# Kernel optimization log

Hardware: AMD Instinct MI355X
Metric: run time of the kernel (lower is better)

The kernel has to match this reference:

```python
import jax, jax.numpy as jnp
import numpy as np

EPS = 0.0001
N, E, DIN, H, DH, C, G = 50000, 800000, 256, 4, 64, 10, 100


def setup_inputs() -> dict:
    key = jax.random.key(0)
    ks = jax.random.split(key, 10)
    x = jax.random.normal(ks[0], (N, DIN), dtype=jnp.float32)
    src = jax.random.randint(ks[1], (E,), 0, N)
    dst = jax.random.randint(ks[2], (E,), 0, N)
    midx = jnp.stack([src, dst]).astype(jnp.int32)
    batch = jnp.sort(jax.random.randint(ks[3], (N,), 0, G)).astype(jnp.int32)
    W_feat = jax.random.normal(ks[4], (DIN, H * DH), dtype=jnp.float32) / np.sqrt(DIN)
    phi = jax.random.normal(ks[5], (H, 2 * DH, 1), dtype=jnp.float32) / np.sqrt(2 * DH)
    W1 = jax.random.normal(ks[6], (H * DH, DH), dtype=jnp.float32) / np.sqrt(H * DH)
    b1 = jnp.zeros((DH,), jnp.float32)
    W2 = jax.random.normal(ks[7], (DH, C), dtype=jnp.float32) / np.sqrt(DH)
    b2 = jnp.zeros((C,), jnp.float32)
    return {"x": x, "midx": midx, "batch": batch, "W_feat": W_feat,
            "phi": phi, "W1": W1, "b1": b1, "W2": W2, "b2": b2}


def reference(x, midx, batch, W_feat, phi, W1, b1, W2, b2):
    src, dst = midx[0], midx[1]
    # per-head node features [N, H, DH]
    h = (x @ W_feat).reshape(-1, H, DH)
    # concat-then-matmul with phi == sum of two half projections (GAT trick)
    phi_s = phi[:, :DH, 0]   # [H, DH]
    phi_d = phi[:, DH:, 0]   # [H, DH]
    a_s = jnp.einsum('nhd,hd->nh', h, phi_s)  # [N, H]
    a_d = jnp.einsum('nhd,hd->nh', h, phi_d)
    w = jax.nn.sigmoid(jax.nn.leaky_relu(a_s[src] + a_d[dst]))  # [E, H]
    msg = (h[dst] * w[:, :, None]).reshape(src.shape[0], H * DH)  # [E, H*DH]
    agg = jax.ops.segment_sum(msg, src, num_segments=x.shape[0])  # scatter_add
    # MLP head (dropout is identity in eval mode)
    z = jax.nn.leaky_relu(agg @ W1 + b1) @ W2 + b2  # [N, C]
    tmp = jnp.exp(z - jnp.max(z, axis=-1, keepdims=True)) + EPS
    preds = tmp / jnp.sum(tmp, axis=-1, keepdims=True)
    # global mean pool over graphs
    sums = jax.ops.segment_sum(preds, batch, num_segments=G)
    cnts = jax.ops.segment_sum(jnp.ones((batch.shape[0],), preds.dtype), batch, num_segments=G)
    yp = sums / cnts[:, None]
    return jnp.log(yp), preds
```

## Files before the change

### kernel.cpp

```cpp
#include <hip/hip_runtime.h>
#include <hip/hip_bf16.h>
#include <cstdint>

#define NN   50000
#define EE   800000
#define DIN_ 256
#define HD_  256
#define DH_  64
#define NH_  4
#define NC_  10
#define NG_  100
#define EPS_ 1e-4f
#define SLOPE_ 0.01f
#define AROW 40
#define CAP_ 48
#define FROW 264

typedef unsigned short ushortT;
typedef __attribute__((ext_vector_type(8))) short short8;
typedef __attribute__((ext_vector_type(4))) float f32x4;

__device__ __forceinline__ float leaky(float x) { return x >= 0.f ? x : SLOPE_ * x; }
__device__ __forceinline__ float sigm(float x)  { return 1.f / (1.f + __expf(-x)); }
__device__ __forceinline__ float b2f(ushortT u) { return __uint_as_float(((unsigned)u) << 16); }
__device__ __forceinline__ ushortT f2b(float f) {
    unsigned u = __float_as_uint(f);
    u += 0x7fffu + ((u >> 16) & 1u);
    return (ushortT)(u >> 16);
}

__global__ void setup_kernel(int* cursor,
                             const float* __restrict__ W, ushortT* __restrict__ wt,
                             const float* __restrict__ W1, ushortT* __restrict__ w1t,
                             const int* __restrict__ batch, int* __restrict__ gstart) {
    int i = blockIdx.x * 256 + threadIdx.x;
    if (i < NN) {
        cursor[i] = 0;
        int b = batch[i];
        int bp = (i == 0) ? -1 : batch[i - 1];
        for (int g = bp + 1; g <= b; g++) gstart[g] = i;
        if (i == NN - 1) {
            for (int g = b + 1; g <= NG_; g++) gstart[g] = NN;
        }
    }
    if (i < DIN_ * HD_) {
        int k = i >> 8, n = i & 255;
        wt[n * DIN_ + k] = f2b(W[i]);
    }
    if (i < 256 * 64) {
        int k = i >> 6, o = i & 63;
        w1t[o * 256 + k] = f2b(W1[i]);
    }
}

__global__ __launch_bounds__(256) void gemm_attn(const float* __restrict__ x,
                                                 const ushortT* __restrict__ wt,
                                                 const float* __restrict__ phi,
                                                 ushortT* __restrict__ hbf,
                                                 float* __restrict__ a_s,
                                                 float* __restrict__ a_d) {
    __shared__ ushortT A_lds[128 * AROW];
    __shared__ ushortT B_lds[128 * AROW];
    const int tid  = threadIdx.x;
    const int wave = tid >> 6, lane = tid & 63;
    const int wm = wave >> 1, wn = wave & 1;
    const int row0 = blockIdx.x * 128;
    const int col0 = blockIdx.y * 128;
    const int q = lane >> 4, l16 = lane & 15;

    f32x4 acc[4][4];
#pragma unroll
    for (int i = 0; i < 4; i++)
#pragma unroll
        for (int j = 0; j < 4; j++) acc[i][j] = (f32x4){0.f, 0.f, 0.f, 0.f};

    const int lm  = tid >> 1;
    const int lko = (tid & 1) * 16;

    for (int k0 = 0; k0 < DIN_; k0 += 32) {
        __syncthreads();
        {
            int gr = row0 + lm;
            float4 a0 = make_float4(0.f,0.f,0.f,0.f), a1 = a0, a2 = a0, a3 = a0;
            if (gr < NN) {
                const float4* xp = (const float4*)(x + (size_t)gr * DIN_ + k0 + lko);
                a0 = xp[0]; a1 = xp[1]; a2 = xp[2]; a3 = xp[3];
            }
            ushortT* ap = &A_lds[lm * AROW + lko];
            *(ushort4*)(ap + 0)  = make_ushort4(f2b(a0.x), f2b(a0.y), f2b(a0.z), f2b(a0.w));
            *(ushort4*)(ap + 4)  = make_ushort4(f2b(a1.x), f2b(a1.y), f2b(a1.z), f2b(a1.w));
            *(ushort4*)(ap + 8)  = make_ushort4(f2b(a2.x), f2b(a2.y), f2b(a2.z), f2b(a2.w));
            *(ushort4*)(ap + 12) = make_ushort4(f2b(a3.x), f2b(a3.y), f2b(a3.z), f2b(a3.w));
        }
        {
            const uint4* wp = (const uint4*)(wt + (size_t)(col0 + lm) * DIN_ + k0 + lko);
            uint4 b0 = wp[0], b1 = wp[1];
            *(uint4*)&B_lds[lm * AROW + lko + 0] = b0;
            *(uint4*)&B_lds[lm * AROW + lko + 8] = b1;
        }
        __syncthreads();

        short8 af[4], bf[4];
#pragma unroll
        for (int mi = 0; mi < 4; mi++)
            af[mi] = *(const short8*)&A_lds[(wm * 64 + mi * 16 + l16) * AROW + q * 8];
#pragma unroll
        for (int ni = 0; ni < 4; ni++)
            bf[ni] = *(const short8*)&B_lds[(wn * 64 + ni * 16 + l16) * AROW + q * 8];
#pragma unroll
        for (int mi = 0; mi < 4; mi++)
#pragma unroll
            for (int ni = 0; ni < 4; ni++)
                acc[mi][ni] = __builtin_amdgcn_mfma_f32_16x16x32_bf16(af[mi], bf[ni], acc[mi][ni], 0, 0, 0);
    }

#pragma unroll
    for (int mi = 0; mi < 4; mi++) {
        int rbase = row0 + wm * 64 + mi * 16 + q * 4;
#pragma unroll
        for (int ni = 0; ni < 4; ni++) {
            int c = col0 + wn * 64 + ni * 16 + l16;
#pragma unroll
            for (int r = 0; r < 4; r++) {
                int gr = rbase + r;
                if (gr < NN) hbf[(size_t)gr * HD_ + c] = f2b(acc[mi][ni][r]);
            }
        }
    }

    int head = blockIdx.y * 2 + wn;
    float phs[4], phd[4];
#pragma unroll
    for (int ni = 0; ni < 4; ni++) {
        phs[ni] = phi[head * 128 + ni * 16 + l16];
        phd[ni] = phi[head * 128 + 64 + ni * 16 + l16];
    }
#pragma unroll
    for (int mi = 0; mi < 4; mi++) {
#pragma unroll
        for (int r = 0; r < 4; r++) {
            float ps = acc[mi][0][r] * phs[0] + acc[mi][1][r] * phs[1]
                     + acc[mi][2][r] * phs[2] + acc[mi][3][r] * phs[3];
            float pd = acc[mi][0][r] * phd[0] + acc[mi][1][r] * phd[1]
                     + acc[mi][2][r] * phd[2] + acc[mi][3][r] * phd[3];
#pragma unroll
            for (int o = 1; o < 16; o <<= 1) {
                ps += __shfl_xor(ps, o);
                pd += __shfl_xor(pd, o);
            }
            if (l16 == 0) {
                int gr = row0 + wm * 64 + mi * 16 + q * 4 + r;
                if (gr < NN) {
                    a_s[gr * 4 + head] = ps;
                    a_d[gr * 4 + head] = pd;
                }
            }
        }
    }
}

__global__ void fill_edges(const int* __restrict__ src, const int* __restrict__ dstA,
                           int* __restrict__ cursor,
                           const float* __restrict__ a_s, const float* __restrict__ a_d,
                           uint4* __restrict__ edges) {
    int e = blockIdx.x * 256 + threadIdx.x;
    if (e >= EE) return;
    int s = src[e], d = dstA[e];
    int slot = atomicAdd(&cursor[s], 1);
    if (slot >= CAP_) return;
    float4 as4 = *(const float4*)(a_s + (size_t)s * 4);
    float4 ad4 = *(const float4*)(a_d + (size_t)d * 4);
    unsigned w01 = (unsigned)f2b(sigm(leaky(as4.x + ad4.x)))
                 | ((unsigned)f2b(sigm(leaky(as4.y + ad4.y))) << 16);
    unsigned w23 = (unsigned)f2b(sigm(leaky(as4.z + ad4.z)))
                 | ((unsigned)f2b(sigm(leaky(as4.w + ad4.w))) << 16);
    edges[(size_t)s * CAP_ + slot] = make_uint4((unsigned)d, w01, w23, 0u);
}

__global__ __launch_bounds__(256) void agg_mlp(const ushortT* __restrict__ hbf,
                                               const int* __restrict__ cursor,
                                               const uint4* __restrict__ edges,
                                               const ushortT* __restrict__ w1t,
                                               const float* __restrict__ b1,
                                               const float* __restrict__ W2,
                                               const float* __restrict__ b2,
                                               float* __restrict__ out) {
    __shared__ ushortT A_lds[16 * FROW];
    __shared__ float z1t[16][68];
    const int tid = threadIdx.x;
    const int wave = tid >> 6, lane = tid & 63;
    const int q = lane >> 4, l16 = lane & 15;
    const int hsel = lane >> 4;
    const int wsh = (hsel & 1) * 16;
    const int n0 = blockIdx.x * 16;
    const ushortT* hbase = hbf + (size_t)lane * 4;

#pragma unroll
    for (int ii = 0; ii < 4; ii++) {
        int ln = wave * 4 + ii;
        int n = n0 + ln;
        int cnt = cursor[n];
        if (cnt > CAP_) cnt = CAP_;
        int e0 = n * CAP_, e1 = e0 + cnt;
        float4 acc = make_float4(0.f, 0.f, 0.f, 0.f);

        int i = e0;
        while (i + 8 <= e1) {
            uint4 ee[8]; ushort4 hh[8]; float ww[8];
#pragma unroll
            for (int j = 0; j < 8; j++) ee[j] = edges[i + j];
#pragma unroll
            for (int j = 0; j < 8; j++) {
                unsigned pair = (hsel & 2) ? ee[j].z : ee[j].y;
                ww[j] = b2f((ushortT)((pair >> wsh) & 0xffffu));
                hh[j] = *(const ushort4*)(hbase + (size_t)ee[j].x * HD_);
            }
#pragma unroll
            for (int j = 0; j < 8; j++) {
                acc.x += b2f(hh[j].x) * ww[j];
                acc.y += b2f(hh[j].y) * ww[j];
                acc.z += b2f(hh[j].z) * ww[j];
                acc.w += b2f(hh[j].w) * ww[j];
            }
            i += 8;
        }
        while (i + 4 <= e1) {
            uint4 ee[4]; ushort4 hh[4]; float ww[4];
#pragma unroll
            for (int j = 0; j < 4; j++) ee[j] = edges[i + j];
#pragma unroll
            for (int j = 0; j < 4; j++) {
                unsigned pair = (hsel & 2) ? ee[j].z : ee[j].y;
                ww[j] = b2f((ushortT)((pair >> wsh) & 0xffffu));
                hh[j] = *(const ushort4*)(hbase + (size_t)ee[j].x * HD_);
            }
#pragma unroll
            for (int j = 0; j < 4; j++) {
                acc.x += b2f(hh[j].x) * ww[j];
                acc.y += b2f(hh[j].y) * ww[j];
                acc.z += b2f(hh[j].z) * ww[j];
                acc.w += b2f(hh[j].w) * ww[j];
            }
            i += 4;
        }
        for (; i < e1; i++) {
            uint4 e = edges[i];
            unsigned pair = (hsel & 2) ? e.z : e.y;
            float s = b2f((ushortT)((pair >> wsh) & 0xffffu));
            ushort4 hv = *(const ushort4*)(hbase + (size_t)e.x * HD_);
            acc.x += b2f(hv.x) * s; acc.y += b2f(hv.y) * s;
            acc.z += b2f(hv.z) * s; acc.w += b2f(hv.w) * s;
        }
        ushort4 o4 = make_ushort4(f2b(acc.x), f2b(acc.y), f2b(acc.z), f2b(acc.w));
        *(ushort4*)&A_lds[ln * FROW + lane * 4] = o4;
    }
    __syncthreads();

    f32x4 macc = (f32x4){0.f, 0.f, 0.f, 0.f};
#pragma unroll
    for (int k0 = 0; k0 < 256; k0 += 32) {
        short8 af = *(const short8*)&A_lds[l16 * FROW + k0 + q * 8];
        short8 bf = *(const short8*)(w1t + (size_t)(wave * 16 + l16) * 256 + k0 + q * 8);
        macc = __builtin_amdgcn_mfma_f32_16x16x32_bf16(af, bf, macc, 0, 0, 0);
    }
    {
        int o = wave * 16 + l16;
        float bb = b1[o];
#pragma unroll
        for (int r = 0; r < 4; r++)
            z1t[q * 4 + r][o] = leaky(macc[r] + bb);
    }
    __syncthreads();

    if (tid < 16) {
        int n = n0 + tid;
        float zc[NC_];
#pragma unroll
        for (int c = 0; c < NC_; c++) zc[c] = b2[c];
        for (int k = 0; k < 64; k += 4) {
            float4 z4 = *(const float4*)&z1t[tid][k];
#pragma unroll
            for (int j = 0; j < 4; j++) {
                float zv = (j == 0) ? z4.x : (j == 1) ? z4.y : (j == 2) ? z4.z : z4.w;
#pragma unroll
                for (int c = 0; c < NC_; c++) zc[c] += zv * W2[(k + j) * NC_ + c];
            }
        }
        float m = zc[0];
#pragma unroll
        for (int c = 1; c < NC_; c++) m = fmaxf(m, zc[c]);
        float ssum = 0.f;
#pragma unroll
        for (int c = 0; c < NC_; c++) { zc[c] = __expf(zc[c] - m) + EPS_; ssum += zc[c]; }
        float inv = 1.f / ssum;
#pragma unroll
        for (int c = 0; c < NC_; c++) out[1000 + (size_t)n * NC_ + c] = zc[c] * inv;
    }
}

__global__ __launch_bounds__(256) void group_mean(const float* __restrict__ preds,
                                                  const int* __restrict__ gstart,
                                                  float* __restrict__ out) {
    __shared__ float red[16][16];
    int g = blockIdx.x;
    int t = threadIdx.x;
    int c = t & 15, chunk = t >> 4;
    int gs = gstart[g], ge = gstart[g + 1];
    float s = 0.f;
    if (c < NC_) {
        for (int n = gs + chunk; n < ge; n += 16) s += preds[(size_t)n * NC_ + c];
    }
    red[chunk][c] = s;
    __syncthreads();
    if (t < NC_) {
        float tot = 0.f;
#pragma unroll
        for (int j = 0; j < 16; j++) tot += red[j][t];
        out[g * NC_ + t] = __logf(tot / (float)(ge - gs));
    }
}

extern "C" void kernel_launch(void* const* d_in, const int* in_sizes, int n_in,
                              void* d_out, int out_size, void* d_ws, size_t ws_size,
                              hipStream_t stream) {
    const float* x      = (const float*)d_in[0];
    const int*   midx   = (const int*)d_in[1];
    const int*   batch  = (const int*)d_in[2];
    const float* W_feat = (const float*)d_in[3];
    const float* phi    = (const float*)d_in[4];
    const float* W1     = (const float*)d_in[5];
    const float* b1     = (const float*)d_in[6];
    const float* W2     = (const float*)d_in[7];
    const float* b2     = (const float*)d_in[8];
    const int* src = midx;
    const int* dst = midx + EE;
    float* out = (float*)d_out;

    char* p = (char*)d_ws;
    auto alloc = [&](size_t bytes) { void* r = (void*)p; p += (bytes + 255) & ~(size_t)255; return r; };
    ushortT* hbf      = (ushortT*)alloc((size_t)NN * HD_ * 2);
    uint4*   edges    = (uint4*)alloc((size_t)NN * CAP_ * 16);
    ushortT* wt       = (ushortT*)alloc((size_t)DIN_ * HD_ * 2);
    ushortT* w1t      = (ushortT*)alloc((size_t)64 * 256 * 2);
    float*   a_s      = (float*)alloc((size_t)NN * 4 * 4);
    float*   a_d      = (float*)alloc((size_t)NN * 4 * 4);
    int*     cursor   = (int*)alloc((size_t)NN * 4);
    int*     gstart   = (int*)alloc((size_t)(NG_ + 1) * 4);

    setup_kernel<<<256, 256, 0, stream>>>(cursor, W_feat, wt, W1, w1t, batch, gstart);
    gemm_attn<<<dim3((NN + 127) / 128, 2), 256, 0, stream>>>(x, wt, phi, hbf, a_s, a_d);
    fill_edges<<<(EE + 255) / 256, 256, 0, stream>>>(src, dst, cursor, a_s, a_d, edges);
    agg_mlp<<<NN / 16, 256, 0, stream>>>(hbf, cursor, edges, w1t, b1, W2, b2, out);
    group_mean<<<NG_, 256, 0, stream>>>(out + 1000, gstart, out);
}
```

Before: 257.4 us.

## Interleave two-node padded gather in aggregation and use MFMA for second MLP layer

Each wave now gathers two destination nodes at a time in padded chunks of 16 edges, issuing all edge and feature loads for both nodes before accumulating. This raises memory-level parallelism and removes the 8/4/1 remainder loops. Padded slots are masked by redirecting to node 0 and zeroing the weight, which adds some wasted loads. The second MLP layer and softmax move from 16 scalar threads to a single bf16 MFMA plus shuffle reductions, using a padded transposed W2 prepared in setup. This adds bf16 rounding of the hidden activations.

```diff
diff --git a/kernel.cpp b/kernel.cpp
--- a/kernel.cpp
+++ b/kernel.cpp
@@ -15,6 +15,7 @@
 #define AROW 40
 #define CAP_ 48
 #define FROW 264
+#define ZROW 80
 
 typedef unsigned short ushortT;
 typedef __attribute__((ext_vector_type(8))) short short8;
@@ -32,6 +33,7 @@
 __global__ void setup_kernel(int* cursor,
                              const float* __restrict__ W, ushortT* __restrict__ wt,
                              const float* __restrict__ W1, ushortT* __restrict__ w1t,
+                             const float* __restrict__ W2, ushortT* __restrict__ w2t,
                              const int* __restrict__ batch, int* __restrict__ gstart) {
     int i = blockIdx.x * 256 + threadIdx.x;
     if (i < NN) {
@@ -50,6 +52,10 @@
     if (i < 256 * 64) {
         int k = i >> 6, o = i & 63;
         w1t[o * 256 + k] = f2b(W1[i]);
+    }
+    if (i < 16 * 64) {
+        int c = i >> 6, k = i & 63;
+        w2t[i] = (c < NC_) ? f2b(W2[k * NC_ + c]) : (ushortT)0;
     }
 }
 
@@ -182,77 +188,86 @@
                                                const uint4* __restrict__ edges,
                                                const ushortT* __restrict__ w1t,
                                                const float* __restrict__ b1,
-                                               const float* __restrict__ W2,
+                                               const ushortT* __restrict__ w2t,
                                                const float* __restrict__ b2,
                                                float* __restrict__ out) {
     __shared__ ushortT A_lds[16 * FROW];
-    __shared__ float z1t[16][68];
+    __shared__ ushortT z1b[16 * ZROW];
     const int tid = threadIdx.x;
-    const int wave = tid >> 6, lane = tid & 63;
+    const int lane = tid & 63;
+    const int wave_u = __builtin_amdgcn_readfirstlane(tid >> 6);
     const int q = lane >> 4, l16 = lane & 15;
-    const int hsel = lane >> 4;
-    const int wsh = (hsel & 1) * 16;
     const int n0 = blockIdx.x * 16;
-    const ushortT* hbase = hbf + (size_t)lane * 4;
-
-#pragma unroll
-    for (int ii = 0; ii < 4; ii++) {
-        int ln = wave * 4 + ii;
-        int n = n0 + ln;
-        int cnt = cursor[n];
-        if (cnt > CAP_) cnt = CAP_;
-        int e0 = n * CAP_, e1 = e0 + cnt;
-        float4 acc = make_float4(0.f, 0.f, 0.f, 0.f);
-
-        int i = e0;
-        while (i + 8 <= e1) {
-            uint4 ee[8]; ushort4 hh[8]; float ww[8];
-#pragma unroll
-            for (int j = 0; j < 8; j++) ee[j] = edges[i + j];
-#pragma unroll
-            for (int j = 0; j < 8; j++) {
-                unsigned pair = (hsel & 2) ? ee[j].z : ee[j].y;
-                ww[j] = b2f((ushortT)((pair >> wsh) & 0xffffu));
-                hh[j] = *(const ushort4*)(hbase + (size_t)ee[j].x * HD_);
-            }
-#pragma unroll
-            for (int j = 0; j < 8; j++) {
-                acc.x += b2f(hh[j].x) * ww[j];
-                acc.y += b2f(hh[j].y) * ww[j];
-                acc.z += b2f(hh[j].z) * ww[j];
-                acc.w += b2f(hh[j].w) * ww[j];
-            }
-            i += 8;
-        }
-        while (i + 4 <= e1) {
-            uint4 ee[4]; ushort4 hh[4]; float ww[4];
-#pragma unroll
-            for (int j = 0; j < 4; j++) ee[j] = edges[i + j];
-#pragma unroll
-            for (int j = 0; j < 4; j++) {
-                unsigned pair = (hsel & 2) ? ee[j].z : ee[j].y;
-                ww[j] = b2f((ushortT)((pair >> wsh) & 0xffffu));
-                hh[j] = *(const ushort4*)(hbase + (size_t)ee[j].x * HD_);
-            }
-#pragma unroll
-            for (int j = 0; j < 4; j++) {
-                acc.x += b2f(hh[j].x) * ww[j];
-                acc.y += b2f(hh[j].y) * ww[j];
-                acc.z += b2f(hh[j].z) * ww[j];
-                acc.w += b2f(hh[j].w) * ww[j];
-            }
-            i += 4;
-        }
-        for (; i < e1; i++) {
-            uint4 e = edges[i];
-            unsigned pair = (hsel & 2) ? e.z : e.y;
-            float s = b2f((ushortT)((pair >> wsh) & 0xffffu));
-            ushort4 hv = *(const ushort4*)(hbase + (size_t)e.x * HD_);
-            acc.x += b2f(hv.x) * s; acc.y += b2f(hv.y) * s;
-            acc.z += b2f(hv.z) * s; acc.w += b2f(hv.w) * s;
-        }
-        ushort4 o4 = make_ushort4(f2b(acc.x), f2b(acc.y), f2b(acc.z), f2b(acc.w));
-        *(ushort4*)&A_lds[ln * FROW + lane * 4] = o4;
+    const char* hbase = (const char*)hbf;
+    const unsigned loff = (unsigned)lane * 8u;
+    const unsigned wsh = (unsigned)(lane >> 4) * 16u;
+
+#pragma unroll 1
+    for (int pp = 0; pp < 2; pp++) {
+        const int nA = n0 + wave_u * 4 + pp * 2;
+        const int nB = nA + 1;
+        int cntA = cursor[nA]; if (cntA > CAP_) cntA = CAP_;
+        int cntB = cursor[nB]; if (cntB > CAP_) cntB = CAP_;
+        const int pcA = (cntA + 15) & ~15;
+        const int pcB = (cntB + 15) & ~15;
+        const int pcm = pcA > pcB ? pcA : pcB;
+        const uint4* erA = edges + (size_t)nA * CAP_;
+        const uint4* erB = edges + (size_t)nB * CAP_;
+        f32x4 accA = (f32x4){0.f, 0.f, 0.f, 0.f};
+        f32x4 accB = (f32x4){0.f, 0.f, 0.f, 0.f};
+#pragma unroll 1
+        for (int i = 0; i < pcm; i += 16) {
+            const bool dA = i < pcA, dB = i < pcB;
+            unsigned eyA[16], ezA[16], eyB[16], ezB[16];
+            ushort4 hA[16], hB[16];
+            if (dA) {
+#pragma unroll
+                for (int j = 0; j < 16; j++) {
+                    uint4 e = erA[i + j];
+                    unsigned sd = (i + j < cntA) ? e.x : 0u;
+                    eyA[j] = e.y; ezA[j] = e.z;
+                    hA[j] = *(const ushort4*)(hbase + ((size_t)sd << 9) + loff);
+                }
+            }
+            if (dB) {
+#pragma unroll
+                for (int j = 0; j < 16; j++) {
+                    uint4 e = erB[i + j];
+                    unsigned sd = (i + j < cntB) ? e.x : 0u;
+                    eyB[j] = e.y; ezB[j] = e.z;
+                    hB[j] = *(const ushort4*)(hbase + ((size_t)sd << 9) + loff);
+                }
+            }
+            if (dA) {
+#pragma unroll
+                for (int j = 0; j < 16; j++) {
+                    unsigned long long wp = (i + j < cntA)
+                        ? ((((unsigned long long)ezA[j]) << 32) | eyA[j]) : 0ull;
+                    float w = b2f((ushortT)((wp >> wsh) & 0xffffu));
+                    accA.x += b2f(hA[j].x) * w;
+                    accA.y += b2f(hA[j].y) * w;
+                    accA.z += b2f(hA[j].z) * w;
+                    accA.w += b2f(hA[j].w) * w;
+                }
+            }
+            if (dB) {
+#pragma unroll
+                for (int j = 0; j < 16; j++) {
+                    unsigned long long wp = (i + j < cntB)
+                        ? ((((unsigned long long)ezB[j]) << 32) | eyB[j]) : 0ull;
+                    float w = b2f((ushortT)((wp >> wsh) & 0xffffu));
+                    accB.x += b2f(hB[j].x) * w;
+                    accB.y += b2f(hB[j].y) * w;
+                    accB.z += b2f(hB[j].z) * w;
+                    accB.w += b2f(hB[j].w) * w;
+                }
+            }
+        }
+        const int lnA = wave_u * 4 + pp * 2;
+        *(ushort4*)&A_lds[lnA * FROW + lane * 4] =
+            make_ushort4(f2b(accA.x), f2b(accA.y), f2b(accA.z), f2b(accA.w));
+        *(ushort4*)&A_lds[(lnA + 1) * FROW + lane * 4] =
+            make_ushort4(f2b(accB.x), f2b(accB.y), f2b(accB.z), f2b(accB.w));
     }
     __syncthreads();
 
@@ -260,41 +275,42 @@
 #pragma unroll
     for (int k0 = 0; k0 < 256; k0 += 32) {
         short8 af = *(const short8*)&A_lds[l16 * FROW + k0 + q * 8];
-        short8 bf = *(const short8*)(w1t + (size_t)(wave * 16 + l16) * 256 + k0 + q * 8);
+        short8 bf = *(const short8*)(w1t + (size_t)(wave_u * 16 + l16) * 256 + k0 + q * 8);
         macc = __builtin_amdgcn_mfma_f32_16x16x32_bf16(af, bf, macc, 0, 0, 0);
     }
     {
-        int o = wave * 16 + l16;
+        int o = wave_u * 16 + l16;
         float bb = b1[o];
 #pragma unroll
         for (int r = 0; r < 4; r++)
-            z1t[q * 4 + r][o] = leaky(macc[r] + bb);
+            z1b[(q * 4 + r) * ZROW + o] = f2b(leaky(macc[r] + bb));
     }
     __syncthreads();
 
-    if (tid < 16) {
-        int n = n0 + tid;
-        float zc[NC_];
-#pragma unroll
-        for (int c = 0; c < NC_; c++) zc[c] = b2[c];
-        for (int k = 0; k < 64; k += 4) {
-            float4 z4 = *(const float4*)&z1t[tid][k];
-#pragma unroll
-            for (int j = 0; j < 4; j++) {
-                float zv = (j == 0) ? z4.x : (j == 1) ? z4.y : (j == 2) ? z4.z : z4.w;
-#pragma unroll
-                for (int c = 0; c < NC_; c++) zc[c] += zv * W2[(k + j) * NC_ + c];
-            }
-        }
-        float m = zc[0];
-#pragma unroll
-        for (int c = 1; c < NC_; c++) m = fmaxf(m, zc[c]);
-        float ssum = 0.f;
-#pragma unroll
-        for (int c = 0; c < NC_; c++) { zc[c] = __expf(zc[c] - m) + EPS_; ssum += zc[c]; }
-        float inv = 1.f / ssum;
-#pragma unroll
-        for (int c = 0; c < NC_; c++) out[1000 + (size_t)n * NC_ + c] = zc[c] * inv;
+    if (wave_u == 0) {
+        f32x4 z2 = (f32x4){0.f, 0.f, 0.f, 0.f};
+#pragma unroll
+        for (int k0 = 0; k0 < 64; k0 += 32) {
+            short8 af = *(const short8*)&z1b[l16 * ZROW + k0 + q * 8];
+            short8 bf = *(const short8*)(w2t + l16 * 64 + k0 + q * 8);
+            z2 = __builtin_amdgcn_mfma_f32_16x16x32_bf16(af, bf, z2, 0, 0, 0);
+        }
+        float bb = (l16 < NC_) ? b2[l16] : 0.f;
+#pragma unroll
+        for (int r = 0; r < 4; r++) {
+            float v = (l16 < NC_) ? (z2[r] + bb) : -1e30f;
+            float m = v;
+#pragma unroll
+            for (int o = 1; o < 16; o <<= 1) m = fmaxf(m, __shfl_xor(m, o));
+            float ev = (l16 < NC_) ? (__expf(v - m) + EPS_) : 0.f;
+            float s = ev;
+#pragma unroll
+            for (int o = 1; o < 16; o <<= 1) s += __shfl_xor(s, o);
+            if (l16 < NC_) {
+                int n = n0 + q * 4 + r;
+                out[1000 + (size_t)n * NC_ + l16] = ev / s;
+            }
+        }
     }
 }
 
@@ -342,14 +358,15 @@
     uint4*   edges    = (uint4*)alloc((size_t)NN * CAP_ * 16);
     ushortT* wt       = (ushortT*)alloc((size_t)DIN_ * HD_ * 2);
     ushortT* w1t      = (ushortT*)alloc((size_t)64 * 256 * 2);
+    ushortT* w2t      = (ushortT*)alloc((size_t)16 * 64 * 2);
     float*   a_s      = (float*)alloc((size_t)NN * 4 * 4);
     float*   a_d      = (float*)alloc((size_t)NN * 4 * 4);
     int*     cursor   = (int*)alloc((size_t)NN * 4);
     int*     gstart   = (int*)alloc((size_t)(NG_ + 1) * 4);
 
-    setup_kernel<<<256, 256, 0, stream>>>(cursor, W_feat, wt, W1, w1t, batch, gstart);
+    setup_kernel<<<256, 256, 0, stream>>>(cursor, W_feat, wt, W1, w1t, W2, w2t, batch, gstart);
     gemm_attn<<<dim3((NN + 127) / 128, 2), 256, 0, stream>>>(x, wt, phi, hbf, a_s, a_d);
     fill_edges<<<(EE + 255) / 256, 256, 0, stream>>>(src, dst, cursor, a_s, a_d, edges);
-    agg_mlp<<<NN / 16, 256, 0, stream>>>(hbf, cursor, edges, w1t, b1, W2, b2, out);
+    agg_mlp<<<NN / 16, 256, 0, stream>>>(hbf, cursor, edges, w1t, b1, w2t, b2, out);
     group_mean<<<NG_, 256, 0, stream>>>(out + 1000, gstart, out);
 }
```

After: 260.7 us. About the same (+1.3%).
